# Performance work log

Hardware: AMD Instinct MI355X
Metric: run time of the kernel (lower is better)

The kernel has to match this reference:

```python
import jax, jax.numpy as jnp
import numpy as np

L, DIM = 8192, 2048

def setup_inputs() -> dict:
    key = jax.random.key(0)
    k1, k2, k3, k4 = jax.random.split(key, 4)
    x = jax.random.normal(k1, (L, DIM), dtype=jnp.float32)
    x_mix_last = jax.random.normal(k2, (DIM,), dtype=jnp.float32)
    factor_param = jax.random.uniform(k3, (DIM,), dtype=jnp.float32)
    W = jax.random.normal(k4, (DIM, DIM), dtype=jnp.float32) * 0.02
    return {"x": x, "x_mix_last": x_mix_last, "factor_param": factor_param, "W": W}

def reference(x, x_mix_last, factor_param, W):
    # x: [L, D] sequence-first, single sequence (no batch dim, as in the torch module)
    seq_len = x.shape[0]
    factor = jax.nn.sigmoid(factor_param)                       # [D]
    exps = jnp.arange(seq_len)[:, None]                         # [L, 1]
    factor_progression = factor[None, :] ** exps                # [L, D], factor^t
    n = 2 * seq_len
    # FFT-based causal convolution of x with the decay kernel factor^t
    fft_prog = jnp.fft.rfft(factor_progression, n=n, axis=0)    # [L+1, D] complex
    fft_x = jnp.fft.rfft(x, n=n, axis=0)                        # [L+1, D] complex
    conv = jnp.fft.irfft(fft_x * fft_prog, n=n, axis=0)[:seq_len]  # [L, D]
    # EMA update: carry decays as factor^(t+1), new input weighted by (1-factor)
    x_mix = x_mix_last[None, :] * factor_progression * factor[None, :] \
            + (1.0 - factor[None, :]) * conv                    # [L, D]
    return x_mix @ W.T                                          # nn.Linear: x @ W^T
```

## Files before the change

kernel.cpp:

```cpp
#include <hip/hip_runtime.h>

#define L_SEQ 8192
#define DIMN  2048
#define CHUNK 64
#define NCHUNK (L_SEQ / CHUNK)

typedef float  f32x4  __attribute__((ext_vector_type(4)));
typedef __bf16 bf16x8 __attribute__((ext_vector_type(8)));

__device__ __forceinline__ unsigned short f2bf(float f) {
    unsigned int u = __float_as_uint(f);
    u += 0x7fffu + ((u >> 16) & 1u);
    return (unsigned short)(u >> 16);
}

__device__ __forceinline__ float sigmoidf_(float v) {
    return 1.0f / (1.0f + __expf(-v));
}

__global__ void scan_carry(const float* __restrict__ x, const float* __restrict__ fp,
                           float* __restrict__ carry) {
    int d = blockIdx.x * 256 + threadIdx.x;
    int c = blockIdx.y;
    float f = sigmoidf_(fp[d]);
    float g = 1.0f - f;
    const float* xp = x + (size_t)c * CHUNK * DIMN + d;
    float h = 0.0f;
#pragma unroll 8
    for (int t = 0; t < CHUNK; ++t) {
        h = fmaf(f, h, g * xp[(size_t)t * DIMN]);
    }
    carry[c * DIMN + d] = h;
}

__global__ void carry_prefix(const float* __restrict__ fp, const float* __restrict__ xml,
                             float* __restrict__ carry) {
    int d = blockIdx.x * 256 + threadIdx.x;
    float f = sigmoidf_(fp[d]);
    float fC = f;
    fC *= fC; fC *= fC; fC *= fC; fC *= fC; fC *= fC; fC *= fC;
    float h = xml[d];
    for (int c = 0; c < NCHUNK; ++c) {
        float local = carry[c * DIMN + d];
        carry[c * DIMN + d] = h;
        h = fmaf(fC, h, local);
    }
}

__global__ void scan_apply(const float* __restrict__ x, const float* __restrict__ fp,
                           const float* __restrict__ carry, unsigned short* __restrict__ xmix) {
    int d = blockIdx.x * 256 + threadIdx.x;
    int c = blockIdx.y;
    float f = sigmoidf_(fp[d]);
    float g = 1.0f - f;
    float h = carry[c * DIMN + d];
    const float* xp = x + (size_t)c * CHUNK * DIMN + d;
    unsigned short* op = xmix + (size_t)c * CHUNK * DIMN + d;
#pragma unroll 8
    for (int t = 0; t < CHUNK; ++t) {
        h = fmaf(f, h, g * xp[(size_t)t * DIMN]);
        op[(size_t)t * DIMN] = f2bf(h);
    }
}

__global__ void conv_w(const float* __restrict__ W, unsigned short* __restrict__ Wb) {
    int i = blockIdx.x * 256 + threadIdx.x;
    float4 v = ((const float4*)W)[i];
    ushort4 o;
    o.x = f2bf(v.x); o.y = f2bf(v.y); o.z = f2bf(v.z); o.w = f2bf(v.w);
    ((ushort4*)Wb)[i] = o;
}

__global__ __launch_bounds__(256) void gemm_bt(
        const unsigned short* __restrict__ A,
        const unsigned short* __restrict__ B,
        float* __restrict__ C) {
    constexpr int N_ = DIMN, K_ = DIMN;
    constexpr int BK = 64;
    __shared__ __align__(16) unsigned short As[128 * BK];
    __shared__ __align__(16) unsigned short Bs[128 * BK];

    int tid  = threadIdx.x;
    int wave = tid >> 6;
    int lane = tid & 63;
    int quad = lane >> 4;
    int l16  = lane & 15;
    int tm = blockIdx.x, tn = blockIdx.y;
    int wm = wave >> 1, wn = wave & 1;

    f32x4 acc[4][4];
#pragma unroll
    for (int i = 0; i < 4; ++i)
#pragma unroll
        for (int j = 0; j < 4; ++j)
            acc[i][j] = (f32x4){0.f, 0.f, 0.f, 0.f};

    const unsigned short* aBase = A + (size_t)(tm * 128) * K_;
    const unsigned short* bBase = B + (size_t)(tn * 128) * K_;

    for (int k0 = 0; k0 < K_; k0 += BK) {
#pragma unroll
        for (int i = 0; i < 4; ++i) {
            int idx = i * 256 + tid;
            int row = idx >> 3, cc = idx & 7;
            __builtin_amdgcn_global_load_lds(
                (const __attribute__((address_space(1))) void*)(aBase + (size_t)row * K_ + k0 + cc * 8),
                (__attribute__((address_space(3))) void*)(As + idx * 8), 16, 0, 0);
        }
#pragma unroll
        for (int i = 0; i < 4; ++i) {
            int idx = i * 256 + tid;
            int row = idx >> 3, cc = idx & 7;
            __builtin_amdgcn_global_load_lds(
                (const __attribute__((address_space(1))) void*)(bBase + (size_t)row * K_ + k0 + cc * 8),
                (__attribute__((address_space(3))) void*)(Bs + idx * 8), 16, 0, 0);
        }
        __syncthreads();

#pragma unroll
        for (int kk = 0; kk < BK; kk += 32) {
            bf16x8 af[4], bg[4];
#pragma unroll
            for (int i = 0; i < 4; ++i) {
                int r = wm * 64 + i * 16 + l16;
                af[i] = *(const bf16x8*)(As + r * BK + kk + quad * 8);
            }
#pragma unroll
            for (int j = 0; j < 4; ++j) {
                int r = wn * 64 + j * 16 + l16;
                bg[j] = *(const bf16x8*)(Bs + r * BK + kk + quad * 8);
            }
#pragma unroll
            for (int i = 0; i < 4; ++i)
#pragma unroll
                for (int j = 0; j < 4; ++j)
                    acc[i][j] = __builtin_amdgcn_mfma_f32_16x16x32_bf16(af[i], bg[j], acc[i][j], 0, 0, 0);
        }
        __syncthreads();
    }

#pragma unroll
    for (int i = 0; i < 4; ++i) {
#pragma unroll
        for (int j = 0; j < 4; ++j) {
            int col = tn * 128 + wn * 64 + j * 16 + l16;
#pragma unroll
            for (int r = 0; r < 4; ++r) {
                int row = tm * 128 + wm * 64 + i * 16 + quad * 4 + r;
                C[(size_t)row * N_ + col] = acc[i][j][r];
            }
        }
    }
}

extern "C" void kernel_launch(void* const* d_in, const int* in_sizes, int n_in,
                              void* d_out, int out_size, void* d_ws, size_t ws_size,
                              hipStream_t stream) {
    const float* x   = (const float*)d_in[0];
    const float* xml = (const float*)d_in[1];
    const float* fp  = (const float*)d_in[2];
    const float* W   = (const float*)d_in[3];
    float* out = (float*)d_out;

    unsigned short* xmix = (unsigned short*)d_ws;
    unsigned short* Wb   = (unsigned short*)((char*)d_ws + (size_t)L_SEQ * DIMN * 2);
    float* carry = (float*)((char*)d_ws + (size_t)L_SEQ * DIMN * 2 + (size_t)DIMN * DIMN * 2);

    scan_carry<<<dim3(DIMN / 256, NCHUNK), 256, 0, stream>>>(x, fp, carry);
    conv_w<<<(DIMN * DIMN / 4) / 256, 256, 0, stream>>>(W, Wb);
    carry_prefix<<<DIMN / 256, 256, 0, stream>>>(fp, xml, carry);
    scan_apply<<<dim3(DIMN / 256, NCHUNK), 256, 0, stream>>>(x, fp, carry, xmix);
    gemm_bt<<<dim3(L_SEQ / 128, DIMN / 128), 256, 0, stream>>>(xmix, Wb, out);
}
```

Before: 245.6 us.

## Fuse scan and weight conversion, vectorize scans, swizzle GEMM LDS tiles

Merges the chunk-carry scan and the weight bf16 conversion into one launch. Both scans now process four channels per thread with float4 loads and ushort4 stores. The carry prefix kernel uses 64-thread blocks and preloads all chunk carries into registers. The GEMM's LDS tiles get an XOR swizzle on the 16-byte column slot to cut bank conflicts on MFMA fragment reads. The cost is fewer threads in the scan kernels (256 blocks), which lowers the parallelism available to hide memory latency.

```diff
diff --git a/kernel.cpp b/kernel.cpp
--- a/kernel.cpp
+++ b/kernel.cpp
@@ -18,57 +18,80 @@
     return 1.0f / (1.0f + __expf(-v));
 }
 
-__global__ void scan_carry(const float* __restrict__ x, const float* __restrict__ fp,
-                           float* __restrict__ carry) {
-    int d = blockIdx.x * 256 + threadIdx.x;
-    int c = blockIdx.y;
-    float f = sigmoidf_(fp[d]);
-    float g = 1.0f - f;
-    const float* xp = x + (size_t)c * CHUNK * DIMN + d;
-    float h = 0.0f;
+__global__ void stage1(const float* __restrict__ x, const float* __restrict__ fp,
+                       const float* __restrict__ W,
+                       float* __restrict__ carry, unsigned short* __restrict__ Wb) {
+    int b = blockIdx.x;
+    if (b < 256) {
+        int cg = b & 1;
+        int c  = b >> 1;
+        int d4 = cg * 256 + threadIdx.x;
+        float4 f4 = ((const float4*)fp)[d4];
+        float fa = sigmoidf_(f4.x), fb = sigmoidf_(f4.y),
+              fc = sigmoidf_(f4.z), fd = sigmoidf_(f4.w);
+        float ga = 1.f - fa, gb = 1.f - fb, gc = 1.f - fc, gd = 1.f - fd;
+        float ha = 0.f, hb = 0.f, hc = 0.f, hd = 0.f;
+        const float4* xp = (const float4*)(x + (size_t)c * CHUNK * DIMN) + d4;
 #pragma unroll 8
-    for (int t = 0; t < CHUNK; ++t) {
-        h = fmaf(f, h, g * xp[(size_t)t * DIMN]);
-    }
-    carry[c * DIMN + d] = h;
-}
-
-__global__ void carry_prefix(const float* __restrict__ fp, const float* __restrict__ xml,
-                             float* __restrict__ carry) {
-    int d = blockIdx.x * 256 + threadIdx.x;
+        for (int t = 0; t < CHUNK; ++t) {
+            float4 v = xp[(size_t)t * (DIMN / 4)];
+            ha = fmaf(fa, ha, ga * v.x);
+            hb = fmaf(fb, hb, gb * v.y);
+            hc = fmaf(fc, hc, gc * v.z);
+            hd = fmaf(fd, hd, gd * v.w);
+        }
+        ((float4*)(carry + (size_t)c * DIMN))[d4] = (float4){ha, hb, hc, hd};
+    } else {
+        int i = (b - 256) * 256 + threadIdx.x;
+        float4 v = ((const float4*)W)[i];
+        ushort4 o;
+        o.x = f2bf(v.x); o.y = f2bf(v.y); o.z = f2bf(v.z); o.w = f2bf(v.w);
+        ((ushort4*)Wb)[i] = o;
+    }
+}
+
+__global__ __launch_bounds__(64) void carry_prefix(const float* __restrict__ fp,
+                                                   const float* __restrict__ xml,
+                                                   float* __restrict__ carry) {
+    int d = blockIdx.x * 64 + threadIdx.x;
     float f = sigmoidf_(fp[d]);
     float fC = f;
     fC *= fC; fC *= fC; fC *= fC; fC *= fC; fC *= fC; fC *= fC;
+    float v[NCHUNK];
+#pragma unroll
+    for (int c = 0; c < NCHUNK; ++c) v[c] = carry[(size_t)c * DIMN + d];
     float h = xml[d];
+#pragma unroll
     for (int c = 0; c < NCHUNK; ++c) {
-        float local = carry[c * DIMN + d];
-        carry[c * DIMN + d] = h;
-        h = fmaf(fC, h, local);
+        carry[(size_t)c * DIMN + d] = h;
+        h = fmaf(fC, h, v[c]);
     }
 }
 
 __global__ void scan_apply(const float* __restrict__ x, const float* __restrict__ fp,
                            const float* __restrict__ carry, unsigned short* __restrict__ xmix) {
-    int d = blockIdx.x * 256 + threadIdx.x;
-    int c = blockIdx.y;
-    float f = sigmoidf_(fp[d]);
-    float g = 1.0f - f;
-    float h = carry[c * DIMN + d];
-    const float* xp = x + (size_t)c * CHUNK * DIMN + d;
-    unsigned short* op = xmix + (size_t)c * CHUNK * DIMN + d;
+    int b = blockIdx.x;
+    int cg = b & 1;
+    int c  = b >> 1;
+    int d4 = cg * 256 + threadIdx.x;
+    float4 f4 = ((const float4*)fp)[d4];
+    float fa = sigmoidf_(f4.x), fb = sigmoidf_(f4.y),
+          fc = sigmoidf_(f4.z), fd = sigmoidf_(f4.w);
+    float ga = 1.f - fa, gb = 1.f - fb, gc = 1.f - fc, gd = 1.f - fd;
+    float4 h0 = ((const float4*)(carry + (size_t)c * DIMN))[d4];
+    float ha = h0.x, hb = h0.y, hc = h0.z, hd = h0.w;
+    const float4* xp = (const float4*)(x + (size_t)c * CHUNK * DIMN) + d4;
+    ushort4* op = (ushort4*)(xmix + (size_t)c * CHUNK * DIMN) + d4;
 #pragma unroll 8
     for (int t = 0; t < CHUNK; ++t) {
-        h = fmaf(f, h, g * xp[(size_t)t * DIMN]);
-        op[(size_t)t * DIMN] = f2bf(h);
-    }
-}
-
-__global__ void conv_w(const float* __restrict__ W, unsigned short* __restrict__ Wb) {
-    int i = blockIdx.x * 256 + threadIdx.x;
-    float4 v = ((const float4*)W)[i];
-    ushort4 o;
-    o.x = f2bf(v.x); o.y = f2bf(v.y); o.z = f2bf(v.z); o.w = f2bf(v.w);
-    ((ushort4*)Wb)[i] = o;
+        float4 v = xp[(size_t)t * (DIMN / 4)];
+        ha = fmaf(fa, ha, ga * v.x);
+        hb = fmaf(fb, hb, gb * v.y);
+        hc = fmaf(fc, hc, gc * v.z);
+        hd = fmaf(fd, hd, gd * v.w);
+        ushort4 o; o.x = f2bf(ha); o.y = f2bf(hb); o.z = f2bf(hc); o.w = f2bf(hd);
+        op[(size_t)t * (DIMN / 4)] = o;
+    }
 }
 
 __global__ __launch_bounds__(256) void gemm_bt(
@@ -102,7 +125,8 @@
 #pragma unroll
         for (int i = 0; i < 4; ++i) {
             int idx = i * 256 + tid;
-            int row = idx >> 3, cc = idx & 7;
+            int row = idx >> 3, slot = idx & 7;
+            int cc = slot ^ (row & 7);
             __builtin_amdgcn_global_load_lds(
                 (const __attribute__((address_space(1))) void*)(aBase + (size_t)row * K_ + k0 + cc * 8),
                 (__attribute__((address_space(3))) void*)(As + idx * 8), 16, 0, 0);
@@ -110,7 +134,8 @@
 #pragma unroll
         for (int i = 0; i < 4; ++i) {
             int idx = i * 256 + tid;
-            int row = idx >> 3, cc = idx & 7;
+            int row = idx >> 3, slot = idx & 7;
+            int cc = slot ^ (row & 7);
             __builtin_amdgcn_global_load_lds(
                 (const __attribute__((address_space(1))) void*)(bBase + (size_t)row * K_ + k0 + cc * 8),
                 (__attribute__((address_space(3))) void*)(Bs + idx * 8), 16, 0, 0);
@@ -123,12 +148,14 @@
 #pragma unroll
             for (int i = 0; i < 4; ++i) {
                 int r = wm * 64 + i * 16 + l16;
-                af[i] = *(const bf16x8*)(As + r * BK + kk + quad * 8);
+                int c0 = (kk >> 3) + quad;
+                af[i] = *(const bf16x8*)(As + r * BK + ((c0 ^ (r & 7)) << 3));
             }
 #pragma unroll
             for (int j = 0; j < 4; ++j) {
                 int r = wn * 64 + j * 16 + l16;
-                bg[j] = *(const bf16x8*)(Bs + r * BK + kk + quad * 8);
+                int c0 = (kk >> 3) + quad;
+                bg[j] = *(const bf16x8*)(Bs + r * BK + ((c0 ^ (r & 7)) << 3));
             }
 #pragma unroll
             for (int i = 0; i < 4; ++i)
@@ -166,9 +193,8 @@
     unsigned short* Wb   = (unsigned short*)((char*)d_ws + (size_t)L_SEQ * DIMN * 2);
     float* carry = (float*)((char*)d_ws + (size_t)L_SEQ * DIMN * 2 + (size_t)DIMN * DIMN * 2);
 
-    scan_carry<<<dim3(DIMN / 256, NCHUNK), 256, 0, stream>>>(x, fp, carry);
-    conv_w<<<(DIMN * DIMN / 4) / 256, 256, 0, stream>>>(W, Wb);
-    carry_prefix<<<DIMN / 256, 256, 0, stream>>>(fp, xml, carry);
-    scan_apply<<<dim3(DIMN / 256, NCHUNK), 256, 0, stream>>>(x, fp, carry, xmix);
+    stage1<<<256 + DIMN * DIMN / 4 / 256, 256, 0, stream>>>(x, fp, W, carry, Wb);
+    carry_prefix<<<DIMN / 64, 64, 0, stream>>>(fp, xml, carry);
+    scan_apply<<<256, 256, 0, stream>>>(x, fp, carry, xmix);
     gemm_bt<<<dim3(L_SEQ / 128, DIMN / 128), 256, 0, stream>>>(xmix, Wb, out);
 }
```

Result: faster. 221.6 us (-9.8%).
